# Kernel optimization log

Measured on AMD Instinct MI355X. Metric: run time of the kernel, lower is better.

The kernel has to match this reference:

```python
import jax, jax.numpy as jnp
import numpy as np

B, T, R, C = 16, 128, 8192, 91   # batch, num_targets, num_reg (proposals), num_classes
RED = 16                          # feature-map stride ('reduction')
IOU_THRESH = 0.7


def setup_inputs() -> dict:
    key = jax.random.key(0)
    ks = jax.random.split(key, 7)
    # Ground-truth boxes [top, left, bottom, right] with strictly positive h/w.
    u = jax.random.uniform(ks[0], (B, T, 4))
    top = u[..., 0] * 400.0
    left = u[..., 1] * 400.0
    h = 32.0 + u[..., 2] * 200.0
    w = 32.0 + u[..., 3] * 200.0
    bboxes = jnp.stack([top, left, top + h, left + w], axis=-1)
    # NMS proposals = jittered copies of random GT boxes, so a realistic fraction has IoU > 0.7.
    tidx = jax.random.randint(ks[1], (B, R), 0, T)
    base = jnp.take_along_axis(bboxes, tidx[:, :, None], axis=1)
    nms_reg = base + jax.random.normal(ks[2], (B, R, 4)) * 4.0
    rcnn_reg = jax.random.normal(ks[3], (B, R, 4)) * 0.1
    rcnn_cls = jax.random.normal(ks[4], (B, R, C))
    nms_cls = jax.random.normal(ks[5], (B, R, 2))  # unused by the loss, kept for API fidelity
    classes = jax.random.randint(ks[6], (B, T), 0, C).astype(jnp.int32)
    return {"nms_reg": nms_reg, "nms_cls": nms_cls, "rcnn_reg": rcnn_reg,
            "rcnn_cls": rcnn_cls, "bboxes": bboxes, "classes": classes, "reduction": RED}


def _iou(a, b):
    # a: [B,1,R,4] proposals, b: [B,T,1,4] targets; box = [top,left,bottom,right]
    it = jnp.maximum(a[..., 0], b[..., 0])
    il = jnp.maximum(a[..., 1], b[..., 1])
    ib = jnp.minimum(a[..., 2], b[..., 2])
    ir = jnp.minimum(a[..., 3], b[..., 3])
    inter = jnp.clip(ib - it, 0.0) * jnp.clip(ir - il, 0.0)
    area_a = (a[..., 2] - a[..., 0]) * (a[..., 3] - a[..., 1])
    area_b = (b[..., 2] - b[..., 0]) * (b[..., 3] - b[..., 1])
    return inter / (area_a + area_b - inter)


def _smooth_l1(x):
    ax = jnp.abs(x)
    return jnp.where(ax < 1.0, 0.5 * x * x, ax - 0.5)


def _masked_mean(v, mask, count):
    return jnp.sum(v * mask) / jnp.maximum(count, 1.0)


def reference(nms_reg, nms_cls, rcnn_reg, rcnn_cls, bboxes, classes, reduction):
    # Pairwise IoU [B, T, R]; original materialized O(B*T*R*4) and O(B*T*R*C) expands.
    iou = _iou(nms_reg[:, None, :, :], bboxes[:, :, None, :])
    # Original sorts along the target dim and takes the last slice == max/argmax.
    max_iou = jnp.max(iou, axis=1)                # [B, R]
    idx = jnp.argmax(iou, axis=1)                 # [B, R] best target per proposal
    max_bboxes = jnp.take_along_axis(bboxes, idx[:, :, None], axis=1)  # [B, R, 4]
    max_classes = jnp.take_along_axis(classes, idx, axis=1)            # [B, R]
    # gather of rcnn_reg / rcnn_cls along the target dim is an identity (they don't depend on it)
    mask = (max_iou > IOU_THRESH).astype(rcnn_reg.dtype)
    count = jnp.sum(mask)

    # CrossEntropyLoss (mean over positives)
    logp = jax.nn.log_softmax(rcnn_cls, axis=-1)
    nll = -jnp.take_along_axis(logp, max_classes[..., None], axis=-1)[..., 0]
    cls_loss = _masked_mean(nll, mask, count)

    # Categorical accuracy over positives
    correct = (jnp.argmax(rcnn_cls, axis=-1) == max_classes).astype(rcnn_reg.dtype)
    accuracy = _masked_mean(correct, mask, count)

    # SmoothL1 on normalized offsets vs rcnn_reg (== masked_reg in original)
    red = jnp.asarray(reduction, rcnn_reg.dtype)
    rounded = jnp.round(max_bboxes / red) * red
    hgt = rounded[..., 2] - rounded[..., 0]
    wid = rounded[..., 3] - rounded[..., 1]
    hgt = jnp.where(hgt == 0.0, 1.0, hgt)  # guard; masked-out rows may have degenerate boxes
    wid = jnp.where(wid == 0.0, 1.0, wid)
    reg_loss = (
        _masked_mean(_smooth_l1(rcnn_reg[..., 0] - (max_bboxes[..., 0] - rounded[..., 0]) / hgt), mask, count)
        + _masked_mean(_smooth_l1(rcnn_reg[..., 1] - (max_bboxes[..., 1] - rounded[..., 1]) / wid), mask, count)
        + _masked_mean(_smooth_l1(rcnn_reg[..., 2] - (max_bboxes[..., 2] - rounded[..., 2]) / hgt), mask, count)
        + _masked_mean(_smooth_l1(rcnn_reg[..., 3] - (max_bboxes[..., 3] - rounded[..., 3]) / wid), mask, count)
    )

    pos = (count > 0.0).astype(rcnn_reg.dtype)  # replaces the .nonzero() branch
    return (cls_loss * pos, reg_loss * pos, accuracy * pos)
```

## Files before the change

kernel.cpp:

```cpp
#include <hip/hip_runtime.h>
#include <hip/hip_bf16.h>

#define NB 16
#define NT 128
#define NR 8192
#define NC 91
#define IOU_TH 0.7f

#define TILES 4
#define GRID_MAIN (NB * NR / (16 * TILES))
#define BLK_PER_B (GRID_MAIN / NB)

__device__ __forceinline__ float fastdiv(float a, float b) {
    return a * __builtin_amdgcn_rcpf(b);
}
__device__ __forceinline__ float smooth_l1(float x) {
    float ax = fabsf(x);
    return ax < 1.0f ? 0.5f * x * x : ax - 0.5f;
}

#define LOADT(S, it_)                                                          \
    {                                                                          \
        const size_t p_ = pbase + (size_t)(it_) * 16;                          \
        pr##S = ((const float4*)nms_reg)[p_];                                  \
        rr##S = ((const float4*)rcnn_reg)[p_];                                 \
        const float* row_ = rcnn_cls + p_ * NC;                                \
        v##S##0 = row_[l];                                                     \
        v##S##1 = row_[l + 16];                                                \
        v##S##2 = row_[l + 32];                                                \
        v##S##3 = row_[l + 48];                                                \
        v##S##4 = row_[l + 64];                                                \
        v##S##5 = v5ok ? row_[c5] : -INFINITY;                                 \
    }

#define PROC(S)                                                                \
    {                                                                          \
        const float area_a = (pr##S.z - pr##S.x) * (pr##S.w - pr##S.y);        \
        unsigned int bu = 0u;                                                  \
        _Pragma("unroll")                                                      \
        for (int j = 0; j < 8; ++j) {                                          \
            const float4 t = tb[j];                                            \
            const float itp = fmaxf(pr##S.x, t.x), il = fmaxf(pr##S.y, t.y);   \
            const float ib  = fminf(pr##S.z, t.z), ir = fminf(pr##S.w, t.w);   \
            const float inter = fmaxf(ib - itp, 0.f) * fmaxf(ir - il, 0.f);    \
            const float iou = fastdiv(inter, (area_a + areaB[j]) - inter);     \
            bu = max(bu, (__float_as_uint(iou) & 0xFFFFFF80u)                  \
                         | (127u - (unsigned int)(l + 16 * j)));               \
        }                                                                      \
        _Pragma("unroll")                                                      \
        for (int mk = 8; mk; mk >>= 1) bu = max(bu, __shfl_xor(bu, mk, 16));   \
        const float best = __uint_as_float(bu & 0xFFFFFF80u);                  \
        if (best > IOU_TH) {                                                   \
            const int bidx = 127 - (int)(bu & 127u);                           \
            const int cls  = scls[bidx];                                       \
            float s = __expf(v##S##0) + __expf(v##S##1) + __expf(v##S##2)      \
                    + __expf(v##S##3) + __expf(v##S##4) + __expf(v##S##5);     \
            unsigned int cb =                                                  \
                (__float_as_uint(v##S##0 + 16.f) & 0xFFFFFF80u)                \
                | (127u - (unsigned int)l);                                    \
            cb = max(cb, (__float_as_uint(v##S##1 + 16.f) & 0xFFFFFF80u)       \
                         | (127u - (unsigned int)(l + 16)));                   \
            cb = max(cb, (__float_as_uint(v##S##2 + 16.f) & 0xFFFFFF80u)       \
                         | (127u - (unsigned int)(l + 32)));                   \
            cb = max(cb, (__float_as_uint(v##S##3 + 16.f) & 0xFFFFFF80u)       \
                         | (127u - (unsigned int)(l + 48)));                   \
            cb = max(cb, (__float_as_uint(v##S##4 + 16.f) & 0xFFFFFF80u)       \
                         | (127u - (unsigned int)(l + 64)));                   \
            cb = max(cb, v5ok ? ((__float_as_uint(v##S##5 + 16.f)              \
                                  & 0xFFFFFF80u)                               \
                                 | (127u - (unsigned int)c5)) : 0u);           \
            _Pragma("unroll")                                                  \
            for (int mk = 8; mk; mk >>= 1) {                                   \
                s += __shfl_xor(s, mk, 16);                                    \
                cb = max(cb, __shfl_xor(cb, mk, 16));                          \
            }                                                                  \
            const int am = 127 - (int)(cb & 127u);                            \
            const int jj = cls >> 4;                                           \
            float val = v##S##0;                                               \
            val = (jj == 1) ? v##S##1 : val;                                   \
            val = (jj == 2) ? v##S##2 : val;                                   \
            val = (jj == 3) ? v##S##3 : val;                                   \
            val = (jj == 4) ? v##S##4 : val;                                   \
            val = (jj == 5) ? v##S##5 : val;                                   \
            const float lc = __shfl(val, cls & 15, 16);                        \
            if (l == 0) {                                                      \
                cnt  += 1.f;                                                   \
                nll  += __logf(s) - lc;                                        \
                corr += (am == cls) ? 1.f : 0.f;                               \
                const float4 bb = sbox[bidx];                                  \
                const float rd0 = rintf(bb.x * rredv) * redv;                  \
                const float rd1 = rintf(bb.y * rredv) * redv;                  \
                const float rd2 = rintf(bb.z * rredv) * redv;                  \
                const float rd3 = rintf(bb.w * rredv) * redv;                  \
                float hgt = rd2 - rd0; if (hgt == 0.f) hgt = 1.f;              \
                float wid = rd3 - rd1; if (wid == 0.f) wid = 1.f;              \
                const float rh = __builtin_amdgcn_rcpf(hgt);                   \
                const float rw = __builtin_amdgcn_rcpf(wid);                   \
                reg += smooth_l1(rr##S.x - (bb.x - rd0) * rh)                  \
                     + smooth_l1(rr##S.y - (bb.y - rd1) * rw)                  \
                     + smooth_l1(rr##S.z - (bb.z - rd2) * rh)                  \
                     + smooth_l1(rr##S.w - (bb.w - rd3) * rw);                 \
            }                                                                  \
        }                                                                      \
    }

__global__ __launch_bounds__(256) void frcnn_main(
    const float* __restrict__ nms_reg,
    const float* __restrict__ rcnn_reg,
    const float* __restrict__ rcnn_cls,
    const float* __restrict__ bboxes,
    const int* __restrict__ classes,
    const int* __restrict__ reduction,
    float4* __restrict__ part)
{
    __shared__ float4 sbox[NT];
    __shared__ int    scls[NT];
    __shared__ float4 sred[4];

    const int b     = blockIdx.x >> 7;
    const int tile0 = (blockIdx.x & (BLK_PER_B - 1)) * TILES;
    const int grp   = threadIdx.x >> 4;
    const int l     = threadIdx.x & 15;

    if (threadIdx.x < NT) {
        sbox[threadIdx.x] = ((const float4*)bboxes)[b * NT + threadIdx.x];
        scls[threadIdx.x] = classes[b * NT + threadIdx.x];
    }
    __syncthreads();

    float4 tb[8];
    float  areaB[8];
    #pragma unroll
    for (int j = 0; j < 8; ++j) {
        tb[j]    = sbox[l + 16 * j];
        areaB[j] = (tb[j].z - tb[j].x) * (tb[j].w - tb[j].y);
    }

    const int rv = *reduction;
    float redv;
    if (rv >= 1 && rv <= 65536) redv = (float)rv;
    else redv = __int_as_float(rv);
    const float rredv = __builtin_amdgcn_rcpf(redv);

    const int  c5   = l + 80;
    const bool v5ok = (c5 < NC);

    const size_t pbase = (size_t)b * NR + tile0 * 16 + grp;

    float4 prA, rrA, prB, rrB;
    float vA0, vA1, vA2, vA3, vA4, vA5;
    float vB0, vB1, vB2, vB3, vB4, vB5;

    float cnt = 0.f, nll = 0.f, reg = 0.f, corr = 0.f;

    LOADT(A, 0)
    LOADT(B, 1)
    PROC(A)
    LOADT(A, 2)
    PROC(B)
    LOADT(B, 3)
    PROC(A)
    PROC(B)

    cnt  += __shfl_down(cnt,  32); nll  += __shfl_down(nll,  32);
    reg  += __shfl_down(reg,  32); corr += __shfl_down(corr, 32);
    cnt  += __shfl_down(cnt,  16); nll  += __shfl_down(nll,  16);
    reg  += __shfl_down(reg,  16); corr += __shfl_down(corr, 16);

    const int lane = threadIdx.x & 63;
    const int w    = threadIdx.x >> 6;
    if (lane == 0) sred[w] = make_float4(cnt, nll, reg, corr);
    __syncthreads();
    if (threadIdx.x == 0) {
        float4 t = make_float4(0.f, 0.f, 0.f, 0.f);
        #pragma unroll
        for (int i = 0; i < 4; ++i) {
            t.x += sred[i].x; t.y += sred[i].y; t.z += sred[i].z; t.w += sred[i].w;
        }
        part[blockIdx.x] = t;
    }
}

__global__ __launch_bounds__(1024) void frcnn_reduce(
    const float4* __restrict__ part, float* __restrict__ out)
{
    __shared__ float4 sw[16];
    float4 s = make_float4(0.f, 0.f, 0.f, 0.f);
    for (int i = threadIdx.x; i < GRID_MAIN; i += 1024) {
        const float4 p = part[i];
        s.x += p.x; s.y += p.y; s.z += p.z; s.w += p.w;
    }
    #pragma unroll
    for (int off = 32; off > 0; off >>= 1) {
        s.x += __shfl_down(s.x, off);
        s.y += __shfl_down(s.y, off);
        s.z += __shfl_down(s.z, off);
        s.w += __shfl_down(s.w, off);
    }
    const int lane = threadIdx.x & 63;
    const int w    = threadIdx.x >> 6;
    if (lane == 0) sw[w] = s;
    __syncthreads();
    if (threadIdx.x == 0) {
        float4 t = make_float4(0.f, 0.f, 0.f, 0.f);
        #pragma unroll
        for (int i = 0; i < 16; ++i) {
            t.x += sw[i].x; t.y += sw[i].y; t.z += sw[i].z; t.w += sw[i].w;
        }
        const float pos   = (t.x > 0.f) ? 1.f : 0.f;
        const float denom = fmaxf(t.x, 1.f);
        out[0] = t.y / denom * pos;
        out[1] = t.z / denom * pos;
        out[2] = t.w / denom * pos;
    }
}

extern "C" void kernel_launch(void* const* d_in, const int* in_sizes, int n_in,
                              void* d_out, int out_size, void* d_ws, size_t ws_size,
                              hipStream_t stream) {
    const float* nms_reg  = (const float*)d_in[0];
    const float* rcnn_reg = (const float*)d_in[2];
    const float* rcnn_cls = (const float*)d_in[3];
    const float* bboxes   = (const float*)d_in[4];
    const int*   classes  = (const int*)d_in[5];
    const int*   red      = (const int*)d_in[6];

    float4* part = (float4*)d_ws;

    frcnn_main<<<GRID_MAIN, 256, 0, stream>>>(nms_reg, rcnn_reg, rcnn_cls, bboxes,
                                              classes, red, part);
    frcnn_reduce<<<1, 1024, 0, stream>>>(part, (float*)d_out);
}
```

Before: 26.13 us.

## Defer positive-row epilogue to a lane-parallel pass and skip unneeded rcnn_reg loads

```diff
diff --git a/kernel.cpp b/kernel.cpp
--- a/kernel.cpp
+++ b/kernel.cpp
@@ -5,9 +5,9 @@
 #define NT 128
 #define NR 8192
 #define NC 91
-#define IOU_TH 0.7f
-
-#define TILES 4
+#define XTH (0.7f / 1.7f)
+
+#define TILES 8
 #define GRID_MAIN (NB * NR / (16 * TILES))
 #define BLK_PER_B (GRID_MAIN / NB)
 
@@ -23,7 +23,6 @@
     {                                                                          \
         const size_t p_ = pbase + (size_t)(it_) * 16;                          \
         pr##S = ((const float4*)nms_reg)[p_];                                  \
-        rr##S = ((const float4*)rcnn_reg)[p_];                                 \
         const float* row_ = rcnn_cls + p_ * NC;                                \
         v##S##0 = row_[l];                                                     \
         v##S##1 = row_[l + 16];                                                \
@@ -33,7 +32,7 @@
         v##S##5 = v5ok ? row_[c5] : -INFINITY;                                 \
     }
 
-#define PROC(S)                                                                \
+#define PROC(S, T)                                                             \
     {                                                                          \
         const float area_a = (pr##S.z - pr##S.x) * (pr##S.w - pr##S.y);        \
         unsigned int bu = 0u;                                                  \
@@ -43,38 +42,27 @@
             const float itp = fmaxf(pr##S.x, t.x), il = fmaxf(pr##S.y, t.y);   \
             const float ib  = fminf(pr##S.z, t.z), ir = fminf(pr##S.w, t.w);   \
             const float inter = fmaxf(ib - itp, 0.f) * fmaxf(ir - il, 0.f);    \
-            const float iou = fastdiv(inter, (area_a + areaB[j]) - inter);     \
-            bu = max(bu, (__float_as_uint(iou) & 0xFFFFFF80u)                  \
+            const float x = fastdiv(inter, area_a + areaB[j]);                 \
+            bu = max(bu, (__float_as_uint(x) & 0xFFFFFF80u)                    \
                          | (127u - (unsigned int)(l + 16 * j)));               \
         }                                                                      \
         _Pragma("unroll")                                                      \
         for (int mk = 8; mk; mk >>= 1) bu = max(bu, __shfl_xor(bu, mk, 16));   \
-        const float best = __uint_as_float(bu & 0xFFFFFF80u);                  \
-        if (best > IOU_TH) {                                                   \
+        float sv = 1.0f, lc = 0.0f;                                            \
+        unsigned int meta = 0u;                                                \
+        if (__uint_as_float(bu & 0xFFFFFF80u) > XTH) {                         \
             const int bidx = 127 - (int)(bu & 127u);                           \
             const int cls  = scls[bidx];                                       \
-            float s = __expf(v##S##0) + __expf(v##S##1) + __expf(v##S##2)      \
-                    + __expf(v##S##3) + __expf(v##S##4) + __expf(v##S##5);     \
-            unsigned int cb =                                                  \
-                (__float_as_uint(v##S##0 + 16.f) & 0xFFFFFF80u)                \
-                | (127u - (unsigned int)l);                                    \
-            cb = max(cb, (__float_as_uint(v##S##1 + 16.f) & 0xFFFFFF80u)       \
-                         | (127u - (unsigned int)(l + 16)));                   \
-            cb = max(cb, (__float_as_uint(v##S##2 + 16.f) & 0xFFFFFF80u)       \
-                         | (127u - (unsigned int)(l + 32)));                   \
-            cb = max(cb, (__float_as_uint(v##S##3 + 16.f) & 0xFFFFFF80u)       \
-                         | (127u - (unsigned int)(l + 48)));                   \
-            cb = max(cb, (__float_as_uint(v##S##4 + 16.f) & 0xFFFFFF80u)       \
-                         | (127u - (unsigned int)(l + 64)));                   \
-            cb = max(cb, v5ok ? ((__float_as_uint(v##S##5 + 16.f)              \
-                                  & 0xFFFFFF80u)                               \
-                                 | (127u - (unsigned int)c5)) : 0u);           \
+            sv = __expf(v##S##0) + __expf(v##S##1) + __expf(v##S##2)           \
+               + __expf(v##S##3) + __expf(v##S##4) + __expf(v##S##5);          \
+            float mv = fmaxf(fmaxf(fmaxf(v##S##0, v##S##1),                    \
+                                   fmaxf(v##S##2, v##S##3)),                   \
+                             fmaxf(v##S##4, v##S##5));                         \
             _Pragma("unroll")                                                  \
             for (int mk = 8; mk; mk >>= 1) {                                   \
-                s += __shfl_xor(s, mk, 16);                                    \
-                cb = max(cb, __shfl_xor(cb, mk, 16));                          \
+                sv += __shfl_xor(sv, mk, 16);                                  \
+                mv  = fmaxf(mv, __shfl_xor(mv, mk, 16));                       \
             }                                                                  \
-            const int am = 127 - (int)(cb & 127u);                            \
             const int jj = cls >> 4;                                           \
             float val = v##S##0;                                               \
             val = (jj == 1) ? v##S##1 : val;                                   \
@@ -82,26 +70,12 @@
             val = (jj == 3) ? v##S##3 : val;                                   \
             val = (jj == 4) ? v##S##4 : val;                                   \
             val = (jj == 5) ? v##S##5 : val;                                   \
-            const float lc = __shfl(val, cls & 15, 16);                        \
-            if (l == 0) {                                                      \
-                cnt  += 1.f;                                                   \
-                nll  += __logf(s) - lc;                                        \
-                corr += (am == cls) ? 1.f : 0.f;                               \
-                const float4 bb = sbox[bidx];                                  \
-                const float rd0 = rintf(bb.x * rredv) * redv;                  \
-                const float rd1 = rintf(bb.y * rredv) * redv;                  \
-                const float rd2 = rintf(bb.z * rredv) * redv;                  \
-                const float rd3 = rintf(bb.w * rredv) * redv;                  \
-                float hgt = rd2 - rd0; if (hgt == 0.f) hgt = 1.f;              \
-                float wid = rd3 - rd1; if (wid == 0.f) wid = 1.f;              \
-                const float rh = __builtin_amdgcn_rcpf(hgt);                   \
-                const float rw = __builtin_amdgcn_rcpf(wid);                   \
-                reg += smooth_l1(rr##S.x - (bb.x - rd0) * rh)                  \
-                     + smooth_l1(rr##S.y - (bb.y - rd1) * rw)                  \
-                     + smooth_l1(rr##S.z - (bb.z - rd2) * rh)                  \
-                     + smooth_l1(rr##S.w - (bb.w - rd3) * rw);                 \
-            }                                                                  \
+            lc = __shfl(val, cls & 15, 16);                                    \
+            meta = (unsigned int)bidx | 128u | ((lc == mv) ? 256u : 0u);       \
         }                                                                      \
+        if (l == 0)                                                            \
+            stash[w][((T) << 2) | (grp & 3)] =                                 \
+                make_float4(__uint_as_float(meta), sv, lc, 0.f);               \
     }
 
 __global__ __launch_bounds__(256) void frcnn_main(
@@ -115,12 +89,14 @@
 {
     __shared__ float4 sbox[NT];
     __shared__ int    scls[NT];
+    __shared__ float4 stash[4][32];
     __shared__ float4 sred[4];
 
-    const int b     = blockIdx.x >> 7;
-    const int tile0 = (blockIdx.x & (BLK_PER_B - 1)) * TILES;
+    const int b     = blockIdx.x / BLK_PER_B;
+    const int tile0 = (blockIdx.x % BLK_PER_B) * TILES;
     const int grp   = threadIdx.x >> 4;
     const int l     = threadIdx.x & 15;
+    const int w     = threadIdx.x >> 6;
 
     if (threadIdx.x < NT) {
         sbox[threadIdx.x] = ((const float4*)bboxes)[b * NT + threadIdx.x];
@@ -145,31 +121,69 @@
     const int  c5   = l + 80;
     const bool v5ok = (c5 < NC);
 
-    const size_t pbase = (size_t)b * NR + tile0 * 16 + grp;
-
-    float4 prA, rrA, prB, rrB;
+    const size_t pbase = (size_t)b * NR + (size_t)tile0 * 16 + grp;
+
+    float4 prA, prB;
     float vA0, vA1, vA2, vA3, vA4, vA5;
     float vB0, vB1, vB2, vB3, vB4, vB5;
 
-    float cnt = 0.f, nll = 0.f, reg = 0.f, corr = 0.f;
-
     LOADT(A, 0)
     LOADT(B, 1)
-    PROC(A)
+    PROC(A, 0)
     LOADT(A, 2)
-    PROC(B)
+    PROC(B, 1)
     LOADT(B, 3)
-    PROC(A)
-    PROC(B)
-
-    cnt  += __shfl_down(cnt,  32); nll  += __shfl_down(nll,  32);
-    reg  += __shfl_down(reg,  32); corr += __shfl_down(corr, 32);
-    cnt  += __shfl_down(cnt,  16); nll  += __shfl_down(nll,  16);
-    reg  += __shfl_down(reg,  16); corr += __shfl_down(corr, 16);
-
-    const int lane = threadIdx.x & 63;
-    const int w    = threadIdx.x >> 6;
-    if (lane == 0) sred[w] = make_float4(cnt, nll, reg, corr);
+    PROC(A, 2)
+    LOADT(A, 4)
+    PROC(B, 3)
+    LOADT(B, 5)
+    PROC(A, 4)
+    LOADT(A, 6)
+    PROC(B, 5)
+    LOADT(B, 7)
+    PROC(A, 6)
+    PROC(B, 7)
+
+    float cnt = 0.f, nll = 0.f, reg = 0.f, corr = 0.f;
+    const int L = threadIdx.x & 63;
+    if (L < 32) {
+        const float4 st = stash[w][L];
+        const unsigned int meta = __float_as_uint(st.x);
+        if (meta & 128u) {
+            const int bidx = (int)(meta & 127u);
+            cnt  = 1.f;
+            corr = (meta & 256u) ? 1.f : 0.f;
+            nll  = __logf(st.y) - st.z;
+
+            const float4 bb = sbox[bidx];
+            const float rd0 = rintf(bb.x * rredv) * redv;
+            const float rd1 = rintf(bb.y * rredv) * redv;
+            const float rd2 = rintf(bb.z * rredv) * redv;
+            const float rd3 = rintf(bb.w * rredv) * redv;
+            float hgt = rd2 - rd0; if (hgt == 0.f) hgt = 1.f;
+            float wid = rd3 - rd1; if (wid == 0.f) wid = 1.f;
+            const float rh = __builtin_amdgcn_rcpf(hgt);
+            const float rw = __builtin_amdgcn_rcpf(wid);
+
+            const int    tl = L >> 2;
+            const size_t p  = (size_t)b * NR + (size_t)(tile0 + tl) * 16
+                            + (unsigned)(4 * w + (L & 3));
+            const float4 rr = ((const float4*)rcnn_reg)[p];
+            reg = smooth_l1(rr.x - (bb.x - rd0) * rh)
+                + smooth_l1(rr.y - (bb.y - rd1) * rw)
+                + smooth_l1(rr.z - (bb.z - rd2) * rh)
+                + smooth_l1(rr.w - (bb.w - rd3) * rw);
+        }
+    }
+
+    #pragma unroll
+    for (int mk = 16; mk; mk >>= 1) {
+        cnt  += __shfl_xor(cnt,  mk, 32);
+        nll  += __shfl_xor(nll,  mk, 32);
+        reg  += __shfl_xor(reg,  mk, 32);
+        corr += __shfl_xor(corr, mk, 32);
+    }
+    if (L == 0) sred[w] = make_float4(cnt, nll, reg, corr);
     __syncthreads();
     if (threadIdx.x == 0) {
         float4 t = make_float4(0.f, 0.f, 0.f, 0.f);
```

Result: faster. 22.92 us (-12.3%).
